# Performance work log

Measured on AMD Instinct MI355X. Metric: run time of the kernel, lower is better.

The kernel has to match this reference:

```python
import jax, jax.numpy as jnp
import numpy as np

TEMP = 34.0   # Dynamic_conv2d default temperature
EPS = 1e-5    # BatchNorm eps


def setup_inputs() -> dict:
    key = jax.random.key(0)
    ks = jax.random.split(key, 4)
    B, Cin, Cout, H, W, K = 8, 32, 16, 256, 256, 4
    hidden = int(Cin * 0.25) + 1  # attention2d hidden planes = 9
    return {
        "x": jax.random.normal(ks[0], (B, Cin, H, W), jnp.float32),
        "weight": jax.random.normal(ks[1], (K, Cout, Cin, 3, 3), jnp.float32) * 0.05,
        "bias": jnp.zeros((K, Cout), jnp.float32),
        "fc1_w": jax.random.normal(ks[2], (hidden, Cin), jnp.float32) * 0.1,
        "fc2_w": jax.random.normal(ks[3], (K, hidden), jnp.float32) * 0.1,
        "fc2_b": jnp.zeros((K,), jnp.float32),
        "bn_gamma": jnp.ones((Cout,), jnp.float32),
        "bn_beta": jnp.zeros((Cout,), jnp.float32),
        "bn_mean": jnp.zeros((Cout,), jnp.float32),
        "bn_var": jnp.ones((Cout,), jnp.float32),
    }


def reference(x, weight, bias, fc1_w, fc2_w, fc2_b, bn_gamma, bn_beta, bn_mean, bn_var):
    xu = jnp.repeat(jnp.repeat(x, 2, axis=2), 2, axis=3)  # [B, Cin, 2H, 2W]

    # 2) attention over K kernels: global avg pool -> 1x1 conv -> relu -> 1x1 conv -> softmax(logits/T)
    pooled = xu.mean(axis=(2, 3))                          # [B, Cin]
    h = jax.nn.relu(pooled @ fc1_w.T)                      # [B, hidden]
    logits = h @ fc2_w.T + fc2_b                           # [B, K]
    attn = jax.nn.softmax(logits / TEMP, axis=-1)          # [B, K]

    # 3) per-sample aggregated conv weights & bias (CondConv-style)
    agg_w = jnp.einsum('bk,koihw->boihw', attn, weight)    # [B, Cout, Cin, 3, 3]
    agg_b = attn @ bias                                    # [B, Cout]

    # 4) per-sample 3x3 conv, stride 1, padding 1 (vmap instead of grouped-conv trick)
    dn = jax.lax.conv_dimension_numbers((1,) + xu.shape[1:], agg_w.shape[1:],
                                        ('NCHW', 'OIHW', 'NCHW'))
    def conv_one(xi, wi, bi):
        y = jax.lax.conv_general_dilated(xi[None], wi, window_strides=(1, 1),
                                         padding=((1, 1), (1, 1)),
                                         dimension_numbers=dn)[0]
        return y + bi[:, None, None]
    y = jax.vmap(conv_one)(xu, agg_w, agg_b)               # [B, Cout, 2H, 2W]

    # 5) BatchNorm (inference with running stats) + ReLU
    scale = bn_gamma / jnp.sqrt(bn_var + EPS)
    shift = bn_beta - bn_mean * scale
    return jax.nn.relu(y * scale[:, None, None] + shift[:, None, None])
```

## Files before the change

### kernel.cpp

```cpp
#include <hip/hip_runtime.h>
#include <hip/hip_bf16.h>

#define B_  8
#define CIN 32
#define COUT 16
#define K_  4
#define HID 9
#define HIN 256
#define WIN 256
#define HW  (HIN * WIN)
#define HOUT 512
#define WOUT 512
#define TEMP 34.0f
#define EPS_ 1e-5f

#define SLAB 1168

typedef float f32x4 __attribute__((ext_vector_type(4)));
typedef __fp16 fp16x2 __attribute__((ext_vector_type(2)));
typedef __fp16 f16x8 __attribute__((ext_vector_type(8)));

union FragB { unsigned u[4]; f16x8 h; };

__device__ inline unsigned pk2(float a, float b) {
    union { fp16x2 f; unsigned u; } x;
    x.f = __builtin_amdgcn_cvt_pkrtz(a, b);
    return x.u;
}
__device__ inline unsigned short f16b(float v) {
    union { __fp16 h; unsigned short u; } x;
    x.h = (__fp16)v;
    return x.u;
}

__global__ __launch_bounds__(256) void pool_kernel(const float* __restrict__ x,
                                                   float* __restrict__ pooled) {
    int bc = blockIdx.x;
    const float4* p = (const float4*)(x + (size_t)bc * HW);
    float s = 0.f;
    for (int i = threadIdx.x; i < HW / 4; i += 256) {
        float4 v = p[i];
        s += v.x + v.y + v.z + v.w;
    }
    #pragma unroll
    for (int off = 32; off > 0; off >>= 1) s += __shfl_down(s, off);
    __shared__ float red[4];
    if ((threadIdx.x & 63) == 0) red[threadIdx.x >> 6] = s;
    __syncthreads();
    if (threadIdx.x == 0)
        pooled[bc] = (red[0] + red[1] + red[2] + red[3]) * (1.f / HW);
}

__global__ __launch_bounds__(256) void attn_weights_kernel(
    const float* __restrict__ pooled, const float* __restrict__ weight,
    const float* __restrict__ bias, const float* __restrict__ fc1_w,
    const float* __restrict__ fc2_w, const float* __restrict__ fc2_b,
    const float* __restrict__ gamma, const float* __restrict__ beta,
    const float* __restrict__ mean, const float* __restrict__ var,
    unsigned short* __restrict__ wpk16, float* __restrict__ bias_eff) {
    int b = blockIdx.x;
    __shared__ float attn[K_];
    if (threadIdx.x == 0) {
        const float* pb = pooled + b * CIN;
        float h[HID];
        for (int j = 0; j < HID; ++j) {
            float s = 0.f;
            for (int c = 0; c < CIN; ++c) s += pb[c] * fc1_w[j * CIN + c];
            h[j] = fmaxf(s, 0.f);
        }
        float lg[K_];
        float mx = -1e30f;
        for (int k = 0; k < K_; ++k) {
            float s = fc2_b[k];
            for (int j = 0; j < HID; ++j) s += h[j] * fc2_w[k * HID + j];
            lg[k] = s * (1.f / TEMP);
            mx = fmaxf(mx, lg[k]);
        }
        float den = 0.f;
        for (int k = 0; k < K_; ++k) { lg[k] = expf(lg[k] - mx); den += lg[k]; }
        for (int k = 0; k < K_; ++k) attn[k] = lg[k] / den;
    }
    __syncthreads();
    float a0 = attn[0], a1 = attn[1], a2 = attn[2], a3v = attn[3];

    for (int p = threadIdx.x; p < COUT * CIN; p += 256) {
        int o = p >> 5, i = p & 31;
        float scale = gamma[o] / sqrtf(var[o] + EPS_);
        const float* w0 = weight + ((size_t)(0 * COUT + o) * CIN + i) * 9;
        const int kstr = COUT * CIN * 9;
        float a3w[9];
        #pragma unroll
        for (int t = 0; t < 9; ++t)
            a3w[t] = scale * (a0 * w0[t] + a1 * w0[kstr + t] +
                              a2 * w0[2 * kstr + t] + a3v * w0[3 * kstr + t]);
        float tmp[2][2][3];
        #pragma unroll
        for (int kx = 0; kx < 3; ++kx) {
            tmp[0][0][kx] = a3w[0 * 3 + kx];
            tmp[0][1][kx] = a3w[1 * 3 + kx] + a3w[2 * 3 + kx];
            tmp[1][0][kx] = a3w[0 * 3 + kx] + a3w[1 * 3 + kx];
            tmp[1][1][kx] = a3w[2 * 3 + kx];
        }
        float w16[16];
        #pragma unroll
        for (int py = 0; py < 2; ++py)
            #pragma unroll
            for (int px = 0; px < 2; ++px)
                #pragma unroll
                for (int u = 0; u < 2; ++u)
                    #pragma unroll
                    for (int v = 0; v < 2; ++v) {
                        const float* t = tmp[py][u];
                        float val = (px == 0) ? (v == 0 ? t[0] : t[1] + t[2])
                                              : (v == 0 ? t[0] + t[1] : t[2]);
                        w16[(py * 2 + px) * 4 + u * 2 + v] = val;
                    }
        const int ks = i >> 3, g = (i >> 1) & 3, hf = i & 1;
        const int l = g * 16 + o;
        #pragma unroll
        for (int par = 0; par < 4; ++par)
            #pragma unroll
            for (int d = 0; d < 4; ++d)
                wpk16[(((size_t)(b * 16 + par * 4 + ks) * 64 + l) * 4 + d) * 2 +
                      hf] = f16b(w16[par * 4 + d]);
    }
    if (threadIdx.x < COUT) {
        int o = threadIdx.x;
        float scale = gamma[o] / sqrtf(var[o] + EPS_);
        float shift = beta[o] - mean[o] * scale;
        float s = a0 * bias[0 * COUT + o] + a1 * bias[1 * COUT + o] +
                  a2 * bias[2 * COUT + o] + a3v * bias[3 * COUT + o];
        bias_eff[b * COUT + o] = s * scale + shift;
    }
}

__global__ __launch_bounds__(256, 2) void conv_kernel(
    const float* __restrict__ x, const unsigned* __restrict__ wpk,
    const float* __restrict__ bias_eff, float* __restrict__ out) {
    const int tile = blockIdx.x;
    const int b = blockIdx.y;
    const int r0 = (tile >> 3) * 32, c0 = (tile & 7) * 32;
    const int tid = threadIdx.x;

    __shared__ unsigned lds32[16 * SLAB];

    const float* xb = x + (size_t)b * CIN * HW;

    for (int i2 = 0; i2 < 16; ++i2) {
        const float* p0 = xb + (size_t)(2 * i2) * HW;
        for (int e = tid; e < 34 * 34; e += 256) {
            int pr = e / 34, pc = e - pr * 34;
            int gr = r0 - 1 + pr, gc = c0 - 1 + pc;
            bool ok = ((unsigned)gr < (unsigned)HIN) &
                      ((unsigned)gc < (unsigned)WIN);
            int off = ok ? (gr * WIN + gc) : 0;
            float v0 = p0[off];
            float v1 = p0[off + HW];
            if (!ok) { v0 = 0.f; v1 = 0.f; }
            lds32[i2 * SLAB + e] = pk2(v0, v1);
        }
    }
    __syncthreads();

    const int w = tid >> 6, lane = tid & 63;
    const int g = lane >> 4, n = lane & 15;

    f16x8 areg[4][4];
    {
        const f16x8* wp = (const f16x8*)wpk + (size_t)b * 1024 + lane;
        #pragma unroll
        for (int par = 0; par < 4; ++par)
            #pragma unroll
            for (int ks = 0; ks < 4; ++ks)
                areg[par][ks] = wp[(par * 4 + ks) * 64];
    }
    float bias4[4];
    #pragma unroll
    for (int q = 0; q < 4; ++q) bias4[q] = bias_eff[b * COUT + g * 4 + q];

    for (int gi = 0; gi < 16; ++gi) {
        const int r = (w << 3) + (gi >> 1);
        const int h = gi & 1;
        const int ab = g * SLAB + r * 34 + (h << 4) + n;

        f32x4 acc[4];
        #pragma unroll
        for (int par = 0; par < 4; ++par)
            acc[par] = (f32x4){0.f, 0.f, 0.f, 0.f};

        #pragma unroll
        for (int ks = 0; ks < 4; ++ks) {
            unsigned nb[3][3];
            #pragma unroll
            for (int du = 0; du < 3; ++du)
                #pragma unroll
                for (int dv = 0; dv < 3; ++dv)
                    nb[du][dv] = lds32[ab + ks * (4 * SLAB) + du * 34 + dv];
            #pragma unroll
            for (int par = 0; par < 4; ++par) {
                const int py = par >> 1, px = par & 1;
                FragB bf;
                bf.u[0] = nb[py][px];
                bf.u[1] = nb[py][px + 1];
                bf.u[2] = nb[py + 1][px];
                bf.u[3] = nb[py + 1][px + 1];
                acc[par] = __builtin_amdgcn_mfma_f32_16x16x32_f16(
                    areg[par][ks], bf.h, acc[par], 0, 0, 0);
            }
        }

        #pragma unroll
        for (int par = 0; par < 4; ++par) {
            const int py = par >> 1, px = par & 1;
            const int y = 2 * (r0 + r) + py;
            const int xg = 2 * (c0 + (h << 4) + n) + px;
            #pragma unroll
            for (int q = 0; q < 4; ++q) {
                float vv = fmaxf(acc[par][q] + bias4[q], 0.f);
                out[((size_t)(b * COUT + g * 4 + q) * HOUT + y) * WOUT + xg] =
                    vv;
            }
        }
    }
}

extern "C" void kernel_launch(void* const* d_in, const int* in_sizes, int n_in,
                              void* d_out, int out_size, void* d_ws, size_t ws_size,
                              hipStream_t stream) {
    const float* x      = (const float*)d_in[0];
    const float* weight = (const float*)d_in[1];
    const float* bias   = (const float*)d_in[2];
    const float* fc1_w  = (const float*)d_in[3];
    const float* fc2_w  = (const float*)d_in[4];
    const float* fc2_b  = (const float*)d_in[5];
    const float* bn_g   = (const float*)d_in[6];
    const float* bn_b   = (const float*)d_in[7];
    const float* bn_m   = (const float*)d_in[8];
    const float* bn_v   = (const float*)d_in[9];
    float* out = (float*)d_out;

    float* ws = (float*)d_ws;
    float*    pooled   = ws;
    float*    bias_eff = ws + 256;
    unsigned* wpk      = (unsigned*)(ws + 512);

    pool_kernel<<<dim3(B_ * CIN), dim3(256), 0, stream>>>(x, pooled);
    attn_weights_kernel<<<dim3(B_), dim3(256), 0, stream>>>(
        pooled, weight, bias, fc1_w, fc2_w, fc2_b, bn_g, bn_b, bn_m, bn_v,
        (unsigned short*)wpk, bias_eff);
    conv_kernel<<<dim3(64, B_), dim3(256), 0, stream>>>(
        x, wpk, bias_eff, out);
}
```

Before: 91.37 us.

## Register-block conv over 8 rows, vectorize stores, widen pool blocks

```diff
diff --git a/kernel.cpp b/kernel.cpp
--- a/kernel.cpp
+++ b/kernel.cpp
@@ -33,22 +33,28 @@
     return x.u;
 }
 
-__global__ __launch_bounds__(256) void pool_kernel(const float* __restrict__ x,
-                                                   float* __restrict__ pooled) {
+__global__ __launch_bounds__(1024) void pool_kernel(const float* __restrict__ x,
+                                                    float* __restrict__ pooled) {
     int bc = blockIdx.x;
     const float4* p = (const float4*)(x + (size_t)bc * HW);
     float s = 0.f;
-    for (int i = threadIdx.x; i < HW / 4; i += 256) {
+    for (int i = threadIdx.x; i < HW / 4; i += 1024) {
         float4 v = p[i];
         s += v.x + v.y + v.z + v.w;
     }
     #pragma unroll
     for (int off = 32; off > 0; off >>= 1) s += __shfl_down(s, off);
-    __shared__ float red[4];
+    __shared__ float red[16];
     if ((threadIdx.x & 63) == 0) red[threadIdx.x >> 6] = s;
     __syncthreads();
-    if (threadIdx.x == 0)
-        pooled[bc] = (red[0] + red[1] + red[2] + red[3]) * (1.f / HW);
+    if (threadIdx.x < 16) {
+        float t = red[threadIdx.x];
+        t += __shfl_down(t, 8);
+        t += __shfl_down(t, 4);
+        t += __shfl_down(t, 2);
+        t += __shfl_down(t, 1);
+        if (threadIdx.x == 0) pooled[bc] = t * (1.f / HW);
+    }
 }
 
 __global__ __launch_bounds__(256) void attn_weights_kernel(
@@ -178,47 +184,53 @@
     #pragma unroll
     for (int q = 0; q < 4; ++q) bias4[q] = bias_eff[b * COUT + g * 4 + q];
 
-    for (int gi = 0; gi < 16; ++gi) {
-        const int r = (w << 3) + (gi >> 1);
-        const int h = gi & 1;
-        const int ab = g * SLAB + r * 34 + (h << 4) + n;
-
-        f32x4 acc[4];
-        #pragma unroll
-        for (int par = 0; par < 4; ++par)
-            acc[par] = (f32x4){0.f, 0.f, 0.f, 0.f};
+    for (int h = 0; h < 2; ++h) {
+        f32x4 acc[8][4];
+        #pragma unroll
+        for (int r8 = 0; r8 < 8; ++r8)
+            #pragma unroll
+            for (int par = 0; par < 4; ++par)
+                acc[r8][par] = (f32x4){0.f, 0.f, 0.f, 0.f};
 
         #pragma unroll
         for (int ks = 0; ks < 4; ++ks) {
-            unsigned nb[3][3];
-            #pragma unroll
-            for (int du = 0; du < 3; ++du)
+            const int base = (ks * 4 + g) * SLAB + (w * 8) * 34 + (h << 4) + n;
+            unsigned nb[10][3];
+            #pragma unroll
+            for (int rr = 0; rr < 10; ++rr)
                 #pragma unroll
                 for (int dv = 0; dv < 3; ++dv)
-                    nb[du][dv] = lds32[ab + ks * (4 * SLAB) + du * 34 + dv];
-            #pragma unroll
-            for (int par = 0; par < 4; ++par) {
-                const int py = par >> 1, px = par & 1;
-                FragB bf;
-                bf.u[0] = nb[py][px];
-                bf.u[1] = nb[py][px + 1];
-                bf.u[2] = nb[py + 1][px];
-                bf.u[3] = nb[py + 1][px + 1];
-                acc[par] = __builtin_amdgcn_mfma_f32_16x16x32_f16(
-                    areg[par][ks], bf.h, acc[par], 0, 0, 0);
-            }
-        }
-
-        #pragma unroll
-        for (int par = 0; par < 4; ++par) {
-            const int py = par >> 1, px = par & 1;
-            const int y = 2 * (r0 + r) + py;
-            const int xg = 2 * (c0 + (h << 4) + n) + px;
-            #pragma unroll
-            for (int q = 0; q < 4; ++q) {
-                float vv = fmaxf(acc[par][q] + bias4[q], 0.f);
-                out[((size_t)(b * COUT + g * 4 + q) * HOUT + y) * WOUT + xg] =
-                    vv;
+                    nb[rr][dv] = lds32[base + rr * 34 + dv];
+            #pragma unroll
+            for (int r8 = 0; r8 < 8; ++r8)
+                #pragma unroll
+                for (int par = 0; par < 4; ++par) {
+                    const int py = par >> 1, px = par & 1;
+                    FragB bf;
+                    bf.u[0] = nb[r8 + py][px];
+                    bf.u[1] = nb[r8 + py][px + 1];
+                    bf.u[2] = nb[r8 + py + 1][px];
+                    bf.u[3] = nb[r8 + py + 1][px + 1];
+                    acc[r8][par] = __builtin_amdgcn_mfma_f32_16x16x32_f16(
+                        areg[par][ks], bf.h, acc[r8][par], 0, 0, 0);
+                }
+        }
+
+        #pragma unroll
+        for (int r8 = 0; r8 < 8; ++r8) {
+            const int rloc = w * 8 + r8;
+            #pragma unroll
+            for (int py = 0; py < 2; ++py) {
+                const int y = 2 * (r0 + rloc) + py;
+                #pragma unroll
+                for (int q = 0; q < 4; ++q) {
+                    float2 st;
+                    st.x = fmaxf(acc[r8][2 * py + 0][q] + bias4[q], 0.f);
+                    st.y = fmaxf(acc[r8][2 * py + 1][q] + bias4[q], 0.f);
+                    *(float2*)&out[((size_t)(b * COUT + g * 4 + q) * HOUT + y) *
+                                       WOUT +
+                                   2 * (c0 + (h << 4) + n)] = st;
+                }
             }
         }
     }
@@ -244,7 +256,7 @@
     float*    bias_eff = ws + 256;
     unsigned* wpk      = (unsigned*)(ws + 512);
 
-    pool_kernel<<<dim3(B_ * CIN), dim3(256), 0, stream>>>(x, pooled);
+    pool_kernel<<<dim3(B_ * CIN), dim3(1024), 0, stream>>>(x, pooled);
     attn_weights_kernel<<<dim3(B_), dim3(256), 0, stream>>>(
         pooled, weight, bias, fc1_w, fc2_w, fc2_b, bn_g, bn_b, bn_m, bn_v,
         (unsigned short*)wpk, bias_eff);
```

Measured after the change: 97.32 us. 6.5% more time.
